# Performance work log

Hardware: AMD Instinct MI355X
Metric: run time of the kernel (lower is better)

## Reference

```python
import jax, jax.numpy as jnp
import numpy as np

N, E = 4096, 131072
IN_DIM, HID, H = 128, 64, 8
D = HID * H          # 512 = d_model
DFF = HID * 4        # 256 (source uses hidden_dim*4, not d_model*4)
NEG_SLOPE = 0.2
LN_EPS = 1e-5


def setup_inputs() -> dict:
    key = jax.random.key(0)
    ks = jax.random.split(key, 24)
    r = lambda i, shp, s=0.05: (jax.random.normal(ks[i], shp, jnp.float32) * s)
    return {
        "x": jax.random.normal(ks[0], (N, IN_DIM), jnp.float32),
        "edge_index": jax.random.randint(ks[1], (2, E), 0, N, dtype=jnp.int32),
        "batch": jnp.zeros((N,), jnp.int32),
        "gat_lin_w": r(2, (D, IN_DIM)),
        "gat_att_src": r(3, (H, HID)),
        "gat_att_dst": r(4, (H, HID)),
        "gat_bias": jnp.zeros((D,), jnp.float32),
        "qkv_w": r(5, (2, 3 * D, D)),
        "qkv_b": jnp.zeros((2, 3 * D), jnp.float32),
        "out_w": r(6, (2, D, D)),
        "out_b": jnp.zeros((2, D), jnp.float32),
        "ln1_g": jnp.ones((2, D), jnp.float32),
        "ln1_b": jnp.zeros((2, D), jnp.float32),
        "ff1_w": r(7, (2, DFF, D)),
        "ff1_b": jnp.zeros((2, DFF), jnp.float32),
        "ff2_w": r(8, (2, D, DFF)),
        "ff2_b": jnp.zeros((2, D), jnp.float32),
        "ln2_g": jnp.ones((2, D), jnp.float32),
        "ln2_b": jnp.zeros((2, D), jnp.float32),
    }


def _layer_norm(x, g, b):
    mu = jnp.mean(x, -1, keepdims=True)
    var = jnp.mean(jnp.square(x - mu), -1, keepdims=True)
    return (x - mu) * jax.lax.rsqrt(var + LN_EPS) * g + b


def _gat(x, edge_index, lin_w, att_src, att_dst, bias):
    # PyG GATConv: linear -> per-edge leaky_relu attention -> softmax over dst -> scatter-add
    h = (x @ lin_w.T).reshape(N, H, HID)                 # [N,H,C]
    loops = jnp.arange(N, dtype=edge_index.dtype)        # add_self_loops=True (PyG default)
    src = jnp.concatenate([edge_index[0], loops])
    dst = jnp.concatenate([edge_index[1], loops])
    a_src = jnp.einsum('nhc,hc->nh', h, att_src)         # [N,H]
    a_dst = jnp.einsum('nhc,hc->nh', h, att_dst)
    e = jax.nn.leaky_relu(a_src[src] + a_dst[dst], NEG_SLOPE)   # [E+N,H]
    emax = jax.ops.segment_max(e, dst, num_segments=N)          # self-loops => no empty segment
    p = jnp.exp(e - emax[dst])
    denom = jax.ops.segment_sum(p, dst, num_segments=N)
    alpha = p / (denom[dst] + 1e-16)                             # [E+N,H]
    msg = alpha[..., None] * h[src]                              # [E+N,H,C]
    out = jax.ops.segment_sum(msg, dst, num_segments=N)         # [N,H,C]
    return out.reshape(N, D) + bias


def _mha(x, w_qkv, b_qkv, w_o, b_o):
    qkv = x @ w_qkv.T + b_qkv                            # [N,3D]
    q, k, v = jnp.split(qkv, 3, axis=-1)
    q = q.reshape(N, H, HID).transpose(1, 0, 2)          # [H,N,c]
    k = k.reshape(N, H, HID).transpose(1, 0, 2)
    v = v.reshape(N, H, HID).transpose(1, 0, 2)
    scores = jnp.einsum('hnc,hmc->hnm', q, k) / jnp.sqrt(jnp.float32(HID))
    attn = jax.nn.softmax(scores, axis=-1)
    o = jnp.einsum('hnm,hmc->hnc', attn, v).transpose(1, 0, 2).reshape(N, D)
    return o @ w_o.T + b_o


def reference(x, edge_index, batch, gat_lin_w, gat_att_src, gat_att_dst, gat_bias,
              qkv_w, qkv_b, out_w, out_b, ln1_g, ln1_b,
              ff1_w, ff1_b, ff2_w, ff2_b, ln2_g, ln2_b):
    h = _gat(x, edge_index, gat_lin_w, gat_att_src, gat_att_dst, gat_bias)
    # TransformerEncoder, 2 post-norm layers, relu FFN, dropout=0; seq_len=N, batch=1
    for i in range(2):
        a = _mha(h, qkv_w[i], qkv_b[i], out_w[i], out_b[i])
        h = _layer_norm(h + a, ln1_g[i], ln1_b[i])
        f = jax.nn.relu(h @ ff1_w[i].T + ff1_b[i]) @ ff2_w[i].T + ff2_b[i]
        h = _layer_norm(h + f, ln2_g[i], ln2_b[i])
    return h
```

## Files before the change

kernel.cpp:

```cpp
#include <hip/hip_runtime.h>
#include <math.h>

#define NN    4096
#define EE    131072
#define ENE   (EE + NN)
#define IND   128
#define HH    8
#define HIDC  64
#define DD    512
#define D3    1536
#define DFF2  256

typedef __attribute__((ext_vector_type(8))) short short8;
typedef __attribute__((ext_vector_type(4))) float f32x4;
typedef __attribute__((ext_vector_type(2))) unsigned int uint2v;

__device__ __forceinline__ float lrelu02(float x) { return x >= 0.f ? x : 0.2f * x; }

__device__ __forceinline__ unsigned short f2bf(float x) {
    unsigned int u = __float_as_uint(x);
    u += 0x7fffu + ((u >> 16) & 1u);
    return (unsigned short)(u >> 16);
}
__device__ __forceinline__ float bf2f(unsigned short u) {
    return __uint_as_float((unsigned int)u << 16);
}
__device__ __forceinline__ unsigned int cvt_pk_bf16(float lo, float hi) {
    unsigned int r;
    asm("v_cvt_pk_bf16_f32 %0, %1, %2" : "=v"(r) : "v"(lo), "v"(hi));
    return r;
}

struct CvtJobs {
    const float* src[6];
    unsigned short* dst[6];
    int n[6];
};

__global__ __launch_bounds__(256) void cvt_many(CvtJobs jb, int total)
{
    int i = (blockIdx.x * 256 + threadIdx.x) * 4;
    if (i >= total) return;
    int s = 0;
    while (i >= jb.n[s]) { i -= jb.n[s]; ++s; }
    float4 v = *(const float4*)(jb.src[s] + i);
    unsigned int lo = (unsigned int)f2bf(v.x) | ((unsigned int)f2bf(v.y) << 16);
    unsigned int hi = (unsigned int)f2bf(v.z) | ((unsigned int)f2bf(v.w) << 16);
    uint2v pk; pk.x = lo; pk.y = hi;
    *(uint2v*)(jb.dst[s] + i) = pk;
}

__global__ __launch_bounds__(256) void gemm_bf16(const unsigned short* __restrict__ A,
                                                 const unsigned short* __restrict__ W,
                                                 const float* __restrict__ bias,
                                                 void* __restrict__ C,
                                                 int M, int K, int N, int flags)
{
    __shared__ __align__(16) unsigned short As[128 * 64];
    __shared__ __align__(16) unsigned short Bs[128 * 64];

    const int t = threadIdx.x, lane = t & 63, w = t >> 6;
    const int wr = w >> 1, wc = w & 1;
    const int bm = blockIdx.y * 128, bn = blockIdx.x * 128;
    const int q = lane & 15, g = lane >> 4;

    f32x4 acc[4][4];
#pragma unroll
    for (int m = 0; m < 4; ++m)
#pragma unroll
        for (int n = 0; n < 4; ++n) acc[m][n] = (f32x4){0.f, 0.f, 0.f, 0.f};

    const int srow = t >> 1, sh = t & 1;
    const unsigned short* Ag = A + (size_t)(bm + srow) * K + sh * 32;
    const unsigned short* Wg = W + (size_t)(bn + srow) * K + sh * 32;
    int wofs[4];
#pragma unroll
    for (int i = 0; i < 4; ++i)
        wofs[i] = srow * 128 + ((((sh * 4 + i) * 16) ^ ((srow & 7) << 4)));

    for (int k0 = 0; k0 < K; k0 += 64) {
        short8 av[4], bv[4];
#pragma unroll
        for (int i = 0; i < 4; ++i) {
            av[i] = *(const short8*)(Ag + k0 + i * 8);
            bv[i] = *(const short8*)(Wg + k0 + i * 8);
        }
        __syncthreads();
#pragma unroll
        for (int i = 0; i < 4; ++i) {
            *(short8*)((char*)As + wofs[i]) = av[i];
            *(short8*)((char*)Bs + wofs[i]) = bv[i];
        }
        __syncthreads();

        short8 af[2][4], bfr[2][4];
#pragma unroll
        for (int m = 0; m < 4; ++m) {
            const int row = wr * 64 + m * 16 + q;
#pragma unroll
            for (int kk = 0; kk < 2; ++kk)
                af[kk][m] = *(const short8*)((const char*)As +
                    row * 128 + ((((kk * 4 + g) * 16) ^ ((row & 7) << 4))));
        }
#pragma unroll
        for (int n = 0; n < 4; ++n) {
            const int row = wc * 64 + n * 16 + q;
#pragma unroll
            for (int kk = 0; kk < 2; ++kk)
                bfr[kk][n] = *(const short8*)((const char*)Bs +
                    row * 128 + ((((kk * 4 + g) * 16) ^ ((row & 7) << 4))));
        }
#pragma unroll
        for (int kk = 0; kk < 2; ++kk)
#pragma unroll
            for (int m = 0; m < 4; ++m)
#pragma unroll
                for (int n = 0; n < 4; ++n)
                    acc[m][n] = __builtin_amdgcn_mfma_f32_16x16x32_bf16(
                        bfr[kk][n], af[kk][m], acc[m][n], 0, 0, 0);
    }

    const int obf = flags & 1, orelu = flags & 2, oqs = flags & 4;
#pragma unroll
    for (int m = 0; m < 4; ++m) {
        const int row = bm + wr * 64 + m * 16 + q;
#pragma unroll
        for (int n = 0; n < 4; ++n) {
            const int col0 = bn + wc * 64 + n * 16 + g * 4;
            f32x4 v = acc[m][n];
            if (bias) {
                float4 bv4 = *(const float4*)(bias + col0);
                v[0] += bv4.x; v[1] += bv4.y; v[2] += bv4.z; v[3] += bv4.w;
            }
            if (oqs && col0 < DD) {
                const float qs = 0.18033688f;
                v[0] *= qs; v[1] *= qs; v[2] *= qs; v[3] *= qs;
            }
            if (orelu) {
                v[0] = fmaxf(v[0], 0.f); v[1] = fmaxf(v[1], 0.f);
                v[2] = fmaxf(v[2], 0.f); v[3] = fmaxf(v[3], 0.f);
            }
            if (obf) {
                uint2v pk;
                pk.x = (unsigned int)f2bf(v[0]) | ((unsigned int)f2bf(v[1]) << 16);
                pk.y = (unsigned int)f2bf(v[2]) | ((unsigned int)f2bf(v[3]) << 16);
                *(uint2v*)((unsigned short*)C + (size_t)row * N + col0) = pk;
            } else {
                float4 o; o.x = v[0]; o.y = v[1]; o.z = v[2]; o.w = v[3];
                *(float4*)((float*)C + (size_t)row * N + col0) = o;
            }
        }
    }
}

__global__ void att_proj(const unsigned short* __restrict__ hlin,
                         const float* __restrict__ att_s,
                         const float* __restrict__ att_d,
                         float* __restrict__ a_src, float* __restrict__ a_dst)
{
    int idx = blockIdx.x * 256 + threadIdx.x;
    if (idx >= NN * HH) return;
    int n = idx >> 3, h = idx & 7;
    const unsigned short* hp = hlin + (size_t)n * DD + h * HIDC;
    const float* as = att_s + h * HIDC;
    const float* ad = att_d + h * HIDC;
    float s1 = 0.f, s2 = 0.f;
#pragma unroll 8
    for (int c = 0; c < HIDC; ++c) {
        float hv = bf2f(hp[c]);
        s1 += hv * as[c]; s2 += hv * ad[c];
    }
    a_src[idx] = s1;
    a_dst[idx] = s2;
}

__global__ void hist_kernel(const int* __restrict__ ei, int* __restrict__ counts)
{
    int i = blockIdx.x * 256 + threadIdx.x;
    if (i >= ENE) return;
    int dst = (i < EE) ? ei[EE + i] : (i - EE);
    atomicAdd(&counts[dst], 1);
}

__global__ __launch_bounds__(1024) void scan_kernel(const int* __restrict__ counts,
                                                    int* __restrict__ offsets)
{
    __shared__ int sums[1024];
    int t = threadIdx.x;
    int v0 = counts[t*4+0], v1 = counts[t*4+1], v2 = counts[t*4+2], v3 = counts[t*4+3];
    sums[t] = v0 + v1 + v2 + v3;
    __syncthreads();
    for (int off = 1; off < 1024; off <<= 1) {
        int x = (t >= off) ? sums[t - off] : 0;
        __syncthreads();
        sums[t] += x;
        __syncthreads();
    }
    int pre = (t > 0) ? sums[t-1] : 0;
    offsets[t*4+0] = pre;
    offsets[t*4+1] = pre + v0;
    offsets[t*4+2] = pre + v0 + v1;
    offsets[t*4+3] = pre + v0 + v1 + v2;
    if (t == 1023) offsets[4096] = sums[1023];
}

__global__ void scatter_kernel(const int* __restrict__ ei, const int* __restrict__ offs,
                               int* __restrict__ cursor, int* __restrict__ src_sorted)
{
    int i = blockIdx.x * 256 + threadIdx.x;
    if (i >= ENE) return;
    int s, d;
    if (i < EE) { s = ei[i]; d = ei[EE + i]; } else { s = d = i - EE; }
    int pos = atomicAdd(&cursor[d], 1);
    src_sorted[offs[d] + pos] = s;
}

__global__ __launch_bounds__(256) void gat_node(const unsigned short* __restrict__ hlin,
                                                const float* __restrict__ a_src,
                                                const float* __restrict__ a_dst,
                                                const int* __restrict__ offs,
                                                const int* __restrict__ src_sorted,
                                                const float* __restrict__ bias,
                                                float* __restrict__ out,
                                                unsigned short* __restrict__ outb)
{
    __shared__ float adst[8];
    __shared__ float emax[8];
    __shared__ float denom[8];
    __shared__ float red[256];
    __shared__ float p_lds[16][8];
    __shared__ int   srcs[16];

    const int n = blockIdx.x, t = threadIdx.x;
    if (t < 8) { adst[t] = a_dst[n * 8 + t]; denom[t] = 0.f; }
    const int off0 = offs[n];
    const int deg  = offs[n+1] - off0;
    __syncthreads();

    const int h = t & 7, slot = t >> 3;
    float mx = -3.0e38f;
    for (int j = slot; j < deg; j += 32) {
        int s = src_sorted[off0 + j];
        mx = fmaxf(mx, a_src[s * 8 + h] + adst[h]);
    }
    red[t] = mx;
    __syncthreads();
    for (int half = 128; half >= 8; half >>= 1) {
        if (t < half) red[t] = fmaxf(red[t], red[t + half]);
        __syncthreads();
    }
    if (t < 8) emax[t] = lrelu02(red[t]);
    __syncthreads();

    float acc0 = 0.f, acc1 = 0.f;
    const int h0 = t >> 6, h1 = (t + 256) >> 6;
    for (int base = 0; base < deg; base += 16) {
        int cnt = min(16, deg - base);
        if (t < cnt * 8) {
            int j = base + (t >> 3);
            int s = src_sorted[off0 + j];
            if ((t & 7) == 0) srcs[t >> 3] = s;
            float x = a_src[s * 8 + (t & 7)] + adst[t & 7];
            float p = __expf(lrelu02(x) - emax[t & 7]);
            p_lds[t >> 3][t & 7] = p;
            atomicAdd(&denom[t & 7], p);
        }
        __syncthreads();
        for (int jj = 0; jj < cnt; ++jj) {
            int s = srcs[jj];
            const unsigned short* hp = hlin + (size_t)s * DD;
            acc0 += p_lds[jj][h0] * bf2f(hp[t]);
            acc1 += p_lds[jj][h1] * bf2f(hp[256 + t]);
        }
        __syncthreads();
    }
    float o0 = acc0 / (denom[h0] + 1e-16f) + bias[t];
    float o1 = acc1 / (denom[h1] + 1e-16f) + bias[256 + t];
    out[(size_t)n * DD + t]        = o0;
    out[(size_t)n * DD + 256 + t]  = o1;
    outb[(size_t)n * DD + t]       = f2bf(o0);
    outb[(size_t)n * DD + 256 + t] = f2bf(o1);
}

#define KVB 128
#define NTT (NN / KVB)

__global__ __launch_bounds__(256) void attn_mfma(const unsigned short* __restrict__ qkv,
                                                 unsigned short* __restrict__ aob)
{
    __shared__ __align__(16) unsigned short Ks0[KVB * 64];
    __shared__ __align__(16) unsigned short Vt0[64 * KVB];
    __shared__ __align__(16) unsigned short Ks1[KVB * 64];
    __shared__ __align__(16) unsigned short Vt1[64 * KVB];

    const int t = threadIdx.x;
    const int w = t >> 6, lane = t & 63;
    const int q15 = lane & 15, g = lane >> 4;

    const int fid = blockIdx.x;
    const int h = fid & 7, qb = fid >> 3;
    const int qbase = qb * 64 + w * 16;

    const unsigned short* qrow = qkv + (size_t)(qbase + q15) * D3 + h * HIDC;
    const short8 qf0 = *(const short8*)(qrow + g * 8);
    const short8 qf1 = *(const short8*)(qrow + 32 + g * 8);

    f32x4 O[4];
#pragma unroll
    for (int db = 0; db < 4; ++db) O[db] = (f32x4){0.f, 0.f, 0.f, 0.f};
    float m_run = -3.0e38f, l_run = 0.f;

    int koff[8][2];
#pragma unroll
    for (int kvb = 0; kvb < 8; ++kvb) {
        const int kr = kvb * 16 + q15;
        koff[kvb][0] = (kr * 64 + g * 8) ^ ((kr & 7) << 3);
        koff[kvb][1] = (kr * 64 + 32 + g * 8) ^ ((kr & 7) << 3);
    }
    int voff[4][4];
#pragma unroll
    for (int db = 0; db < 4; ++db) {
        const int vr = db * 16 + q15;
#pragma unroll
        for (int ks = 0; ks < 4; ++ks)
            voff[db][ks] = (vr * KVB + ks * 32 + g * 8) ^ ((vr & 7) << 3);
    }
    const int kr_s = t >> 1, sh = t & 1;
    const int kq = t & 31, dg = t >> 5;
    const int slot4 = (kq >> 3) * 32 + (kq & 3) * 8 + ((kq >> 2) & 1) * 4;
    int kwoff[4];
#pragma unroll
    for (int i = 0; i < 4; ++i)
        kwoff[i] = (kr_s * 64 + (sh * 4 + i) * 8) ^ ((kr_s & 7) << 3);
    int vwoff[8];
#pragma unroll
    for (int i = 0; i < 8; ++i) {
        const int d = dg * 8 + i;
        vwoff[i] = (d * KVB + slot4) ^ ((d & 7) << 3);
    }
    const unsigned short* Kg = qkv + (size_t)kr_s * D3 + DD + h * HIDC + sh * 32;
    const unsigned short* Vg = qkv + (size_t)(4 * kq) * D3 + 2 * DD + h * HIDC + dg * 8;

    short8 kreg[4], vreg[4];

    auto LOAD_KV = [&](int kb) {
        const size_t off = (size_t)kb * KVB * D3;
#pragma unroll
        for (int i = 0; i < 4; ++i) kreg[i] = *(const short8*)(Kg + off + i * 8);
#pragma unroll
        for (int jj = 0; jj < 4; ++jj) vreg[jj] = *(const short8*)(Vg + off + (size_t)jj * D3);
    };
    auto WRITE_KV = [&](unsigned short* KD, unsigned short* VD) {
#pragma unroll
        for (int i = 0; i < 4; ++i)
            *(short8*)&KD[kwoff[i]] = kreg[i];
        const unsigned int* w0 = (const unsigned int*)&vreg[0];
        const unsigned int* w1 = (const unsigned int*)&vreg[1];
        const unsigned int* w2 = (const unsigned int*)&vreg[2];
        const unsigned int* w3 = (const unsigned int*)&vreg[3];
#pragma unroll
        for (int i = 0; i < 8; ++i) {
            unsigned int a0 = w0[i >> 1], a1 = w1[i >> 1], a2 = w2[i >> 1], a3 = w3[i >> 1];
            unsigned int pk01, pk23;
            if (i & 1) {
                pk01 = (a1 & 0xffff0000u) | (a0 >> 16);
                pk23 = (a3 & 0xffff0000u) | (a2 >> 16);
            } else {
                pk01 = (a1 << 16) | (a0 & 0xffffu);
                pk23 = (a3 << 16) | (a2 & 0xffffu);
            }
            uint2v pk; pk.x = pk01; pk.y = pk23;
            *(uint2v*)&VD[vwoff[i]] = pk;
        }
    };

    auto TILE = [&](int kb, const unsigned short* BK, const unsigned short* BV,
                    unsigned short* NK, unsigned short* NV) {
        const int kbn = kb + 1;
        if (kbn < NTT) LOAD_KV(kbn);

        f32x4 st[8];
        __builtin_amdgcn_s_setprio(1);
#pragma unroll
        for (int kvb = 0; kvb < 8; ++kvb) {
            const short8 kf0 = *(const short8*)&BK[koff[kvb][0]];
            const short8 kf1 = *(const short8*)&BK[koff[kvb][1]];
            f32x4 acc = (f32x4){0.f, 0.f, 0.f, 0.f};
            acc = __builtin_amdgcn_mfma_f32_16x16x32_bf16(kf0, qf0, acc, 0, 0, 0);
            acc = __builtin_amdgcn_mfma_f32_16x16x32_bf16(kf1, qf1, acc, 0, 0, 0);
            st[kvb] = acc;
        }
        __builtin_amdgcn_s_setprio(0);

        float pmax = -3.0e38f;
#pragma unroll
        for (int kvb = 0; kvb < 8; ++kvb) {
            float m01 = fmaxf(st[kvb][0], st[kvb][1]);
            float m23 = fmaxf(st[kvb][2], st[kvb][3]);
            pmax = fmaxf(pmax, fmaxf(m01, m23));
        }
        pmax = fmaxf(pmax, __shfl_xor(pmax, 16, 64));
        pmax = fmaxf(pmax, __shfl_xor(pmax, 32, 64));
        if (!__all(pmax <= m_run + 11.f)) {
            const float mnew = fmaxf(m_run, pmax);
            const float f = exp2f(m_run - mnew);
            l_run *= f;
#pragma unroll
            for (int db = 0; db < 4; ++db) O[db] *= f;
            m_run = mnew;
        }

        short8 pf[4];
        float ls = 0.f;
#pragma unroll
        for (int ks = 0; ks < 4; ++ks) {
            float e0 = exp2f(st[2*ks  ][0] - m_run), e1 = exp2f(st[2*ks  ][1] - m_run);
            float e2 = exp2f(st[2*ks  ][2] - m_run), e3 = exp2f(st[2*ks  ][3] - m_run);
            float e4 = exp2f(st[2*ks+1][0] - m_run), e5 = exp2f(st[2*ks+1][1] - m_run);
            float e6 = exp2f(st[2*ks+1][2] - m_run), e7 = exp2f(st[2*ks+1][3] - m_run);
            ls += ((e0 + e1) + (e2 + e3)) + ((e4 + e5) + (e6 + e7));
            union { unsigned int u[4]; short8 s8; } pu;
            pu.u[0] = cvt_pk_bf16(e0, e1);
            pu.u[1] = cvt_pk_bf16(e2, e3);
            pu.u[2] = cvt_pk_bf16(e4, e5);
            pu.u[3] = cvt_pk_bf16(e6, e7);
            pf[ks] = pu.s8;
        }
        ls += __shfl_xor(ls, 16, 64);
        ls += __shfl_xor(ls, 32, 64);
        l_run += ls;

        __builtin_amdgcn_s_setprio(1);
#pragma unroll
        for (int db = 0; db < 4; ++db) {
#pragma unroll
            for (int ks = 0; ks < 4; ++ks) {
                const short8 vf = *(const short8*)&BV[voff[db][ks]];
                O[db] = __builtin_amdgcn_mfma_f32_16x16x32_bf16(vf, pf[ks], O[db], 0, 0, 0);
            }
        }
        __builtin_amdgcn_s_setprio(0);

        if (kbn < NTT) {
            WRITE_KV(NK, NV);
            __syncthreads();
        }
    };

    LOAD_KV(0);
    WRITE_KV(Ks0, Vt0);
    __syncthreads();

    for (int kb = 0; kb < NTT; kb += 2) {
        TILE(kb,     Ks0, Vt0, Ks1, Vt1);
        TILE(kb + 1, Ks1, Vt1, Ks0, Vt0);
    }

    const float linv = 1.f / l_run;
#pragma unroll
    for (int db = 0; db < 4; ++db) {
        uint2v pk;
        pk.x = (unsigned int)f2bf(O[db][0] * linv) | ((unsigned int)f2bf(O[db][1] * linv) << 16);
        pk.y = (unsigned int)f2bf(O[db][2] * linv) | ((unsigned int)f2bf(O[db][3] * linv) << 16);
        *(uint2v*)&aob[(size_t)(qbase + q15) * DD + h * HIDC + db * 16 + g * 4] = pk;
    }
}

__global__ __launch_bounds__(256) void ln_fused(const float* __restrict__ hin,
                                                const float* __restrict__ dlt,
                                                const float* __restrict__ g,
                                                const float* __restrict__ b,
                                                float* __restrict__ out,
                                                unsigned short* __restrict__ outb)
{
    __shared__ float red[256];
    const int r = blockIdx.x, t = threadIdx.x;
    const size_t base = (size_t)r * DD;
    float v0 = hin[base + t] + dlt[base + t];
    float v1 = hin[base + 256 + t] + dlt[base + 256 + t];
    red[t] = v0 + v1;
    __syncthreads();
    for (int off = 128; off > 0; off >>= 1) { if (t < off) red[t] += red[t + off]; __syncthreads(); }
    float mu = red[0] * (1.f / 512.f);
    __syncthreads();
    float d0 = v0 - mu, d1 = v1 - mu;
    red[t] = d0 * d0 + d1 * d1;
    __syncthreads();
    for (int off = 128; off > 0; off >>= 1) { if (t < off) red[t] += red[t + off]; __syncthreads(); }
    float rs = rsqrtf(red[0] * (1.f / 512.f) + 1e-5f);
    float o0 = d0 * rs * g[t] + b[t];
    float o1 = d1 * rs * g[256 + t] + b[256 + t];
    out[base + t]       = o0;
    out[base + 256 + t] = o1;
    if (outb) {
        outb[base + t]       = f2bf(o0);
        outb[base + 256 + t] = f2bf(o1);
    }
}

extern "C" void kernel_launch(void* const* d_in, const int* in_sizes, int n_in,
                              void* d_out, int out_size, void* d_ws, size_t ws_size,
                              hipStream_t stream)
{
    (void)in_sizes; (void)n_in; (void)out_size; (void)ws_size;

    const float* x        = (const float*)d_in[0];
    const int*   ei       = (const int*)  d_in[1];
    const float* lin_w    = (const float*)d_in[3];
    const float* att_src  = (const float*)d_in[4];
    const float* att_dst  = (const float*)d_in[5];
    const float* gat_bias = (const float*)d_in[6];
    const float* qkv_w    = (const float*)d_in[7];
    const float* qkv_b    = (const float*)d_in[8];
    const float* out_w    = (const float*)d_in[9];
    const float* out_b    = (const float*)d_in[10];
    const float* ln1_g    = (const float*)d_in[11];
    const float* ln1_b    = (const float*)d_in[12];
    const float* ff1_w    = (const float*)d_in[13];
    const float* ff1_b    = (const float*)d_in[14];
    const float* ff2_w    = (const float*)d_in[15];
    const float* ff2_b    = (const float*)d_in[16];
    const float* ln2_g    = (const float*)d_in[17];
    const float* ln2_b    = (const float*)d_in[18];

    char* wsb = (char*)d_ws;
    size_t o = 0;
    auto alloc = [&](size_t bytes) { char* p = wsb + o; o += (bytes + 255) & ~(size_t)255; return p; };

    unsigned short* hlin_bf = (unsigned short*)alloc((size_t)NN * DD * 2);
    unsigned short* hbf     = (unsigned short*)alloc((size_t)NN * DD * 2);
    unsigned short* qkv16   = (unsigned short*)alloc((size_t)NN * D3 * 2);
    unsigned short* aob     = (unsigned short*)alloc((size_t)NN * DD * 2);
    unsigned short* ff1obf  = (unsigned short*)alloc((size_t)NN * DFF2 * 2);
    float* hcur  = (float*)alloc((size_t)NN * DD * 4);
    float* tmp1  = (float*)alloc((size_t)NN * DD * 4);
    float* a_src = (float*)alloc((size_t)NN * HH * 4);
    float* a_dst = (float*)alloc((size_t)NN * HH * 4);
    int* counts     = (int*)alloc(NN * 4);
    int* cursor     = (int*)alloc(NN * 4);
    int* offsets    = (int*)alloc((NN + 1) * 4);
    int* src_sorted = (int*)alloc(ENE * 4);
    unsigned short* xbf    = (unsigned short*)alloc((size_t)NN * IND * 2);
    unsigned short* linwbf = (unsigned short*)alloc((size_t)DD * IND * 2);
    unsigned short* qkvwbf = (unsigned short*)alloc((size_t)2 * D3 * DD * 2);
    unsigned short* outwbf = (unsigned short*)alloc((size_t)2 * DD * DD * 2);
    unsigned short* ff1wbf = (unsigned short*)alloc((size_t)2 * DFF2 * DD * 2);
    unsigned short* ff2wbf = (unsigned short*)alloc((size_t)2 * DD * DFF2 * 2);

    CvtJobs jb;
    jb.src[0] = x;      jb.dst[0] = xbf;    jb.n[0] = NN * IND;
    jb.src[1] = lin_w;  jb.dst[1] = linwbf; jb.n[1] = DD * IND;
    jb.src[2] = qkv_w;  jb.dst[2] = qkvwbf; jb.n[2] = 2 * D3 * DD;
    jb.src[3] = out_w;  jb.dst[3] = outwbf; jb.n[3] = 2 * DD * DD;
    jb.src[4] = ff1_w;  jb.dst[4] = ff1wbf; jb.n[4] = 2 * DFF2 * DD;
    jb.src[5] = ff2_w;  jb.dst[5] = ff2wbf; jb.n[5] = 2 * DD * DFF2;
    int cvt_total = jb.n[0]+jb.n[1]+jb.n[2]+jb.n[3]+jb.n[4]+jb.n[5];
    cvt_many<<<(cvt_total/4 + 255)/256, 256, 0, stream>>>(jb, cvt_total);

    hipMemsetAsync(counts, 0, 2 * NN * sizeof(int), stream);
    gemm_bf16<<<dim3(DD/128, NN/128), 256, 0, stream>>>(xbf, linwbf, nullptr, hlin_bf,
                                                        NN, IND, DD, 1);
    att_proj<<<(NN*HH + 255)/256, 256, 0, stream>>>(hlin_bf, att_src, att_dst, a_src, a_dst);
    hist_kernel<<<(ENE + 255)/256, 256, 0, stream>>>(ei, counts);
    scan_kernel<<<1, 1024, 0, stream>>>(counts, offsets);
    scatter_kernel<<<(ENE + 255)/256, 256, 0, stream>>>(ei, offsets, cursor, src_sorted);
    gat_node<<<NN, 256, 0, stream>>>(hlin_bf, a_src, a_dst, offsets, src_sorted, gat_bias,
                                     hcur, hbf);

    for (int i = 0; i < 2; ++i) {
        gemm_bf16<<<dim3(D3/128, NN/128), 256, 0, stream>>>(hbf, qkvwbf + (size_t)i*D3*DD,
                                                            qkv_b + (size_t)i*D3, qkv16,
                                                            NN, DD, D3, 1 | 4);
        attn_mfma<<<dim3(NN/64 * HH), 256, 0, stream>>>(qkv16, aob);
        gemm_bf16<<<dim3(DD/128, NN/128), 256, 0, stream>>>(aob, outwbf + (size_t)i*DD*DD,
                                                            out_b + (size_t)i*DD, tmp1,
                                                            NN, DD, DD, 0);
        ln_fused<<<NN, 256, 0, stream>>>(hcur, tmp1, ln1_g + (size_t)i*DD, ln1_b + (size_t)i*DD,
                                         hcur, hbf);
        gemm_bf16<<<dim3(DFF2/128, NN/128), 256, 0, stream>>>(hbf, ff1wbf + (size_t)i*DFF2*DD,
                                                              ff1_b + (size_t)i*DFF2, ff1obf,
                                                              NN, DD, DFF2, 1 | 2);
        gemm_bf16<<<dim3(DD/128, NN/128), 256, 0, stream>>>(ff1obf, ff2wbf + (size_t)i*DD*DFF2,
                                                            ff2_b + (size_t)i*DD, tmp1,
                                                            NN, DFF2, DD, 0);
        float* outp = (i == 1) ? (float*)d_out : hcur;
        unsigned short* outbp = (i == 1) ? nullptr : hbf;
        ln_fused<<<NN, 256, 0, stream>>>(hcur, tmp1, ln2_g + (size_t)i*DD, ln2_b + (size_t)i*DD,
                                         outp, outbp);
    }
}
```

Measured before the change: 403.8 us.

## Compute softmax row sums via extra ones-row MFMA and use max3/perm ops

The attention kernel extends the V^T tile in LDS with 16 extra rows, the first filled with bf16 ones, so an additional MFMA block computes the softmax denominator alongside P·V. This replaces the per-tile VALU sum and its cross-lane shuffles. The max reduction now uses v_max3_f32, and the V transpose packing uses byte-permute instructions. The trade is four extra MFMAs per tile, more LDS, and a denominator summed from bf16-rounded probabilities, which slightly changes numerics.

```diff
diff --git a/kernel.cpp b/kernel.cpp
--- a/kernel.cpp
+++ b/kernel.cpp
@@ -28,6 +28,11 @@
 __device__ __forceinline__ unsigned int cvt_pk_bf16(float lo, float hi) {
     unsigned int r;
     asm("v_cvt_pk_bf16_f32 %0, %1, %2" : "=v"(r) : "v"(lo), "v"(hi));
+    return r;
+}
+__device__ __forceinline__ float max3f(float a, float b, float c) {
+    float r;
+    asm("v_max3_f32 %0, %1, %2, %3" : "=v"(r) : "v"(a), "v"(b), "v"(c));
     return r;
 }
 
@@ -289,9 +294,9 @@
                                                  unsigned short* __restrict__ aob)
 {
     __shared__ __align__(16) unsigned short Ks0[KVB * 64];
-    __shared__ __align__(16) unsigned short Vt0[64 * KVB];
+    __shared__ __align__(16) unsigned short Vt0[80 * KVB];
     __shared__ __align__(16) unsigned short Ks1[KVB * 64];
-    __shared__ __align__(16) unsigned short Vt1[64 * KVB];
+    __shared__ __align__(16) unsigned short Vt1[80 * KVB];
 
     const int t = threadIdx.x;
     const int w = t >> 6, lane = t & 63;
@@ -308,7 +313,8 @@
     f32x4 O[4];
 #pragma unroll
     for (int db = 0; db < 4; ++db) O[db] = (f32x4){0.f, 0.f, 0.f, 0.f};
-    float m_run = -3.0e38f, l_run = 0.f;
+    f32x4 O5 = (f32x4){0.f, 0.f, 0.f, 0.f};
+    float m_run = -3.0e38f;
 
     int koff[8][2];
 #pragma unroll
@@ -324,6 +330,12 @@
 #pragma unroll
         for (int ks = 0; ks < 4; ++ks)
             voff[db][ks] = (vr * KVB + ks * 32 + g * 8) ^ ((vr & 7) << 3);
+    }
+    int voffE[4];
+#pragma unroll
+    for (int ks = 0; ks < 4; ++ks) {
+        const int rv = 64 + q15;
+        voffE[ks] = (rv * KVB + ks * 32 + g * 8) ^ ((rv & 7) << 3);
     }
     const int kr_s = t >> 1, sh = t & 1;
     const int kq = t & 31, dg = t >> 5;
@@ -360,16 +372,10 @@
         const unsigned int* w3 = (const unsigned int*)&vreg[3];
 #pragma unroll
         for (int i = 0; i < 8; ++i) {
-            unsigned int a0 = w0[i >> 1], a1 = w1[i >> 1], a2 = w2[i >> 1], a3 = w3[i >> 1];
-            unsigned int pk01, pk23;
-            if (i & 1) {
-                pk01 = (a1 & 0xffff0000u) | (a0 >> 16);
-                pk23 = (a3 & 0xffff0000u) | (a2 >> 16);
-            } else {
-                pk01 = (a1 << 16) | (a0 & 0xffffu);
-                pk23 = (a3 << 16) | (a2 & 0xffffu);
-            }
-            uint2v pk; pk.x = pk01; pk.y = pk23;
+            const unsigned int sel = (i & 1) ? 0x07060302u : 0x05040100u;
+            uint2v pk;
+            pk.x = __builtin_amdgcn_perm(w1[i >> 1], w0[i >> 1], sel);
+            pk.y = __builtin_amdgcn_perm(w3[i >> 1], w2[i >> 1], sel);
             *(uint2v*)&VD[vwoff[i]] = pk;
         }
     };
@@ -392,33 +398,40 @@
         }
         __builtin_amdgcn_s_setprio(0);
 
-        float pmax = -3.0e38f;
-#pragma unroll
-        for (int kvb = 0; kvb < 8; ++kvb) {
-            float m01 = fmaxf(st[kvb][0], st[kvb][1]);
-            float m23 = fmaxf(st[kvb][2], st[kvb][3]);
-            pmax = fmaxf(pmax, fmaxf(m01, m23));
-        }
+        float pm0 = max3f(st[0][0], st[0][1], st[0][2]);
+        float pm1 = max3f(st[0][3], st[1][0], st[1][1]);
+        float pm2 = max3f(st[1][2], st[1][3], st[2][0]);
+        float pm3 = max3f(st[2][1], st[2][2], st[2][3]);
+        float pm4 = max3f(st[3][0], st[3][1], st[3][2]);
+        float pm5 = max3f(st[3][3], st[4][0], st[4][1]);
+        float pm6 = max3f(st[4][2], st[4][3], st[5][0]);
+        float pm7 = max3f(st[5][1], st[5][2], st[5][3]);
+        float pm8 = max3f(st[6][0], st[6][1], st[6][2]);
+        float pm9 = max3f(st[6][3], st[7][0], st[7][1]);
+        float pmA = max3f(st[7][2], st[7][3], pm0);
+        float q0 = max3f(pm1, pm2, pm3);
+        float q1 = max3f(pm4, pm5, pm6);
+        float q2 = max3f(pm7, pm8, pm9);
+        float pmax = max3f(q0, q1, q2);
+        pmax = fmaxf(pmax, pmA);
         pmax = fmaxf(pmax, __shfl_xor(pmax, 16, 64));
         pmax = fmaxf(pmax, __shfl_xor(pmax, 32, 64));
         if (!__all(pmax <= m_run + 11.f)) {
             const float mnew = fmaxf(m_run, pmax);
             const float f = exp2f(m_run - mnew);
-            l_run *= f;
 #pragma unroll
             for (int db = 0; db < 4; ++db) O[db] *= f;
+            O5 *= f;
             m_run = mnew;
         }
 
         short8 pf[4];
-        float ls = 0.f;
 #pragma unroll
         for (int ks = 0; ks < 4; ++ks) {
             float e0 = exp2f(st[2*ks  ][0] - m_run), e1 = exp2f(st[2*ks  ][1] - m_run);
             float e2 = exp2f(st[2*ks  ][2] - m_run), e3 = exp2f(st[2*ks  ][3] - m_run);
             float e4 = exp2f(st[2*ks+1][0] - m_run), e5 = exp2f(st[2*ks+1][1] - m_run);
             float e6 = exp2f(st[2*ks+1][2] - m_run), e7 = exp2f(st[2*ks+1][3] - m_run);
-            ls += ((e0 + e1) + (e2 + e3)) + ((e4 + e5) + (e6 + e7));
             union { unsigned int u[4]; short8 s8; } pu;
             pu.u[0] = cvt_pk_bf16(e0, e1);
             pu.u[1] = cvt_pk_bf16(e2, e3);
@@ -426,9 +439,6 @@
             pu.u[3] = cvt_pk_bf16(e6, e7);
             pf[ks] = pu.s8;
         }
-        ls += __shfl_xor(ls, 16, 64);
-        ls += __shfl_xor(ls, 32, 64);
-        l_run += ls;
 
         __builtin_amdgcn_s_setprio(1);
 #pragma unroll
@@ -439,6 +449,11 @@
                 O[db] = __builtin_amdgcn_mfma_f32_16x16x32_bf16(vf, pf[ks], O[db], 0, 0, 0);
             }
         }
+#pragma unroll
+        for (int ks = 0; ks < 4; ++ks) {
+            const short8 vfE = *(const short8*)&BV[voffE[ks]];
+            O5 = __builtin_amdgcn_mfma_f32_16x16x32_bf16(vfE, pf[ks], O5, 0, 0, 0);
+        }
         __builtin_amdgcn_s_setprio(0);
 
         if (kbn < NTT) {
@@ -447,6 +462,16 @@
         }
     };
 
+    {
+        const int d = 64 + (t >> 4), c = (t & 15) * 8;
+        short8 iv;
+#pragma unroll
+        for (int i = 0; i < 8; ++i)
+            iv[i] = (short)((d == 64) ? 0x3F80 : 0);
+        const int ofs = (d * KVB + c) ^ ((d & 7) << 3);
+        *(short8*)&Vt0[ofs] = iv;
+        *(short8*)&Vt1[ofs] = iv;
+    }
     LOAD_KV(0);
     WRITE_KV(Ks0, Vt0);
     __syncthreads();
@@ -456,7 +481,8 @@
         TILE(kb + 1, Ks1, Vt1, Ks0, Vt0);
     }
 
-    const float linv = 1.f / l_run;
+    const float lsum = __shfl(O5[0], q15, 64);
+    const float linv = 1.f / lsum;
 #pragma unroll
     for (int db = 0; db < 4; ++db) {
         uint2v pk;
```

Result: faster. 383.1 us (-5.1%).
